# Performance work log

Measured on AMD Instinct MI355X. Metric: run time of the kernel, lower is better.

## Reference

```python
import jax, jax.numpy as jnp
import numpy as np

IN_DIM = 128
DIM = 32
N_HEADS = 4
EPS = 1e-5


def setup_inputs() -> dict:
    key = jax.random.key(0)
    ks = jax.random.split(key, 8)
    b, L = 1, 320
    s = 0.02
    return {
        "z": jax.random.normal(ks[0], (b, L, L, IN_DIM), dtype=jnp.float32),
        "ln_g": jnp.ones((IN_DIM,), jnp.float32),
        "ln_b": jnp.zeros((IN_DIM,), jnp.float32),
        "Wqkv": jax.random.normal(ks[1], (IN_DIM, DIM * 3 * N_HEADS), jnp.float32) * s,
        "Wpair": jax.random.normal(ks[2], (IN_DIM, N_HEADS), jnp.float32) * s,
        "Wgate": jax.random.normal(ks[3], (IN_DIM, N_HEADS * DIM), jnp.float32) * s,
        "bgate": jnp.zeros((N_HEADS * DIM,), jnp.float32),
        "Wout": jax.random.normal(ks[4], (N_HEADS * DIM, IN_DIM), jnp.float32) * s,
        "bout": jnp.zeros((IN_DIM,), jnp.float32),
    }


def _layernorm(x, g, b):
    m = jnp.mean(x, axis=-1, keepdims=True)
    v = jnp.mean(jnp.square(x - m), axis=-1, keepdims=True)
    return (x - m) * jax.lax.rsqrt(v + EPS) * g + b


def reference(z, ln_g, ln_b, Wqkv, Wpair, Wgate, bgate, Wout, bout):
    B, L, _, _ = z.shape
    zn = _layernorm(z, ln_g, ln_b)  # [b,i,j,c]
    qkv = zn @ Wqkv                 # [b,i,j,3*h*d]
    q, k, v = jnp.split(qkv, 3, axis=-1)
    rs = lambda t: t.reshape(B, L, L, N_HEADS, DIM)
    q, k, v = rs(q), rs(k), rs(v)
    pair_bias = zn @ Wpair          # [b,i,j,h]
    gate = jax.nn.sigmoid(zn @ Wgate + bgate)  # [b,i,j,h*d]
    scale = DIM ** 0.5
    # row-wise: attend over j within each row r=i
    # scores: [b,r,i,j,h]; bias broadcast over r
    scores = jnp.einsum('brihd,brjhd->brijh', q, k / scale)
    scores = scores + pair_bias[:, None]
    attn = jax.nn.softmax(scores, axis=3)
    out = jnp.einsum('brijh,brjhd->brihd', attn, v)  # [b,r,i,h,d]
    out = out.reshape(B, L, L, N_HEADS * DIM)
    return (gate * out) @ Wout + bout
```

## Files before the change

kernel.cpp:

```cpp
#include <hip/hip_runtime.h>
#include <math.h>


#define LL 320
#define CC 128
#define NPOS (LL*LL)

typedef __attribute__((ext_vector_type(8))) __bf16 bf16x8;
typedef __attribute__((ext_vector_type(4))) __bf16 bf16x4;
typedef __attribute__((ext_vector_type(4))) float f32x4;

#define MFMA16(a,b,c) __builtin_amdgcn_mfma_f32_16x16x32_bf16(a,b,c,0,0,0)

__device__ __forceinline__ int swz(int m, int kc) {
    return m*128 + ((kc ^ (m & 7)) << 3);
}

__global__ __launch_bounds__(128) void k_wprep(
    const float* __restrict__ Wqkv, const float* __restrict__ Wgate,
    const float* __restrict__ Wout, __bf16* __restrict__ wT)
{
    const int n = blockIdx.x, t = threadIdx.x;
    float v;
    if (n < 384)      v = Wqkv[(size_t)t*384 + n] * (n < 128 ? 0.17677669529663687f : 1.f);
    else if (n < 512) v = Wgate[(size_t)t*128 + (n-384)];
    else              v = Wout[(size_t)t*128 + (n-512)];
    wT[(size_t)n*128 + t] = (__bf16)v;
}

__global__ __launch_bounds__(512) void k_ln_proj(
    const float* __restrict__ z, const float* __restrict__ lng, const float* __restrict__ lnb,
    const __bf16* __restrict__ wT, const float* __restrict__ Wpair,
    const float* __restrict__ bgate,
    __bf16* __restrict__ qkvb, float* __restrict__ pairT, float* __restrict__ gate)
{
    __shared__ __bf16 As[128*128];
    __shared__ __bf16 Bs[128*128];
    const int t = threadIdx.x;
    const int posBase = blockIdx.x * 128;

    {
        const int r0 = t >> 2, q = t & 3;
        const float* zp = z + (size_t)(posBase + r0)*CC + q*32;
        float v[32];
        float s = 0.f, sq = 0.f;
#pragma unroll
        for (int i = 0; i < 8; ++i) {
            float4 f = ((const float4*)zp)[i];
            v[4*i+0]=f.x; v[4*i+1]=f.y; v[4*i+2]=f.z; v[4*i+3]=f.w;
            s  += f.x + f.y + f.z + f.w;
            sq += f.x*f.x + f.y*f.y + f.z*f.z + f.w*f.w;
        }
        s  += __shfl_xor(s, 1);  sq += __shfl_xor(sq, 1);
        s  += __shfl_xor(s, 2);  sq += __shfl_xor(sq, 2);
        const float mean = s * (1.f/128.f);
        const float var  = sq * (1.f/128.f) - mean*mean;
        const float rstd = rsqrtf(var + 1e-5f);
        const float4* g4 = (const float4*)(lng + q*32);
        const float4* b4 = (const float4*)(lnb + q*32);
#pragma unroll
        for (int i = 0; i < 8; ++i) {
            float4 gg = g4[i], bb = b4[i];
            v[4*i+0] = (v[4*i+0]-mean)*rstd*gg.x + bb.x;
            v[4*i+1] = (v[4*i+1]-mean)*rstd*gg.y + bb.y;
            v[4*i+2] = (v[4*i+2]-mean)*rstd*gg.z + bb.z;
            v[4*i+3] = (v[4*i+3]-mean)*rstd*gg.w + bb.w;
        }
#pragma unroll
        for (int i2 = 0; i2 < 8; ++i2) {
            bf16x4 pk;
            pk[0] = (__bf16)v[4*i2+0]; pk[1] = (__bf16)v[4*i2+1];
            pk[2] = (__bf16)v[4*i2+2]; pk[3] = (__bf16)v[4*i2+3];
            *(bf16x4*)&As[swz(r0, q*4 + (i2>>1)) + (i2&1)*4] = pk;
        }
        float pc0=0.f, pc1=0.f, pc2=0.f, pc3=0.f;
#pragma unroll 8
        for (int kk = 0; kk < 32; ++kk) {
            float4 wp = *(const float4*)&Wpair[(q*32 + kk)*4];
            pc0 += v[kk]*wp.x; pc1 += v[kk]*wp.y; pc2 += v[kk]*wp.z; pc3 += v[kk]*wp.w;
        }
        pc0 += __shfl_xor(pc0,1); pc0 += __shfl_xor(pc0,2);
        pc1 += __shfl_xor(pc1,1); pc1 += __shfl_xor(pc1,2);
        pc2 += __shfl_xor(pc2,1); pc2 += __shfl_xor(pc2,2);
        pc3 += __shfl_xor(pc3,1); pc3 += __shfl_xor(pc3,2);
        if (q == 0) {
            pairT[0*(size_t)NPOS + posBase + r0] = pc0;
            pairT[1*(size_t)NPOS + posBase + r0] = pc1;
            pairT[2*(size_t)NPOS + posBase + r0] = pc2;
            pairT[3*(size_t)NPOS + posBase + r0] = pc3;
        }
    }

    const int lane = t & 63, wv = t >> 6;
    const int l15 = lane & 15, quad = lane >> 4;
    const int m0 = wv * 16;
    const int srow = t >> 2, skc0 = (t & 3) * 4;

    for (int ch = 0; ch < 4; ++ch) {
        __syncthreads();
        {
            const __bf16* src = wT + (size_t)(ch*128 + srow)*128;
#pragma unroll
            for (int j = 0; j < 4; ++j)
                *(bf16x8*)&Bs[swz(srow, skc0 + j)] = *(const bf16x8*)(src + (skc0 + j)*8);
        }
        __syncthreads();

        f32x4 acc[8] = {};
#pragma unroll
        for (int kstep = 0; kstep < 4; ++kstep) {
            bf16x8 aA = *(const bf16x8*)&As[swz(m0 + l15, kstep*4 + quad)];
#pragma unroll
            for (int nt = 0; nt < 8; ++nt) {
                bf16x8 bB = *(const bf16x8*)&Bs[swz(nt*16 + l15, kstep*4 + quad)];
                acc[nt] = MFMA16(aA, bB, acc[nt]);
            }
        }

        if (ch < 3) {
#pragma unroll
            for (int reg = 0; reg < 4; ++reg) {
                __bf16* qp = qkvb + (size_t)(posBase + m0 + quad*4 + reg)*384 + ch*128 + l15;
#pragma unroll
                for (int nt = 0; nt < 8; ++nt)
                    qp[nt*16] = (__bf16)acc[nt][reg];
            }
        } else {
#pragma unroll
            for (int reg = 0; reg < 4; ++reg) {
                float* gp = gate + (size_t)(posBase + m0 + quad*4 + reg)*128 + l15;
#pragma unroll
                for (int nt = 0; nt < 8; ++nt) {
                    float x = acc[nt][reg] + bgate[nt*16 + l15];
                    gp[nt*16] = 1.f/(1.f + __expf(-x));
                }
            }
        }
    }
}

__global__ __launch_bounds__(256) void k_attn(
    const __bf16* __restrict__ qkvb, const float* __restrict__ pairT,
    const float* __restrict__ gate, __bf16* __restrict__ attb)
{
    __shared__ __bf16 Ks[64*32];
    __shared__ __bf16 Vt[32*72];
    __shared__ __bf16 Ps[4][16*72];

    const int t = threadIdx.x, wave = t >> 6, lane = t & 63;
    const int l15 = lane & 15, quad = lane >> 4;
    const int bx = blockIdx.x, r = bx / 5, itile = bx - r*5, h = blockIdx.y;
    const int iw0 = itile*64 + wave*16;

    bf16x8 aq = *(const bf16x8*)(qkvb + (size_t)(r*LL + iw0 + l15)*384 + h*32 + quad*8);

    f32x4 o0 = {0.f,0.f,0.f,0.f}, o1 = {0.f,0.f,0.f,0.f};
    float lp[4] = {0.f,0.f,0.f,0.f};
    const float* bp = pairT + (size_t)h*NPOS + (size_t)(iw0 + quad*4)*LL + l15;

    const int srow = t >> 2, sq4 = t & 3;
    const __bf16* kvbase = qkvb + (size_t)(r*LL)*384 + h*32 + sq4*8;
    __bf16* pw = &Ps[wave][0];

    for (int j0 = 0; j0 < LL; j0 += 64) {
        __syncthreads();
        {
            const __bf16* kp = kvbase + (size_t)(j0 + srow)*384 + 128;
            *(bf16x8*)&Ks[srow*32 + sq4*8] = *(const bf16x8*)kp;
            bf16x8 vv = *(const bf16x8*)(kp + 128);
#pragma unroll
            for (int i = 0; i < 8; ++i) Vt[(sq4*8 + i)*72 + srow] = vv[i];
        }
        __syncthreads();

        const f32x4 zero = {0.f,0.f,0.f,0.f};
        f32x4 s[4];
#pragma unroll
        for (int nt = 0; nt < 4; ++nt) {
            bf16x8 bk = *(const bf16x8*)&Ks[(nt*16 + l15)*32 + quad*8];
            s[nt] = MFMA16(aq, bk, zero);
        }
#pragma unroll
        for (int reg = 0; reg < 4; ++reg) {
            const float* bpr = bp + (size_t)reg*LL + j0;
            float rs = 0.f;
#pragma unroll
            for (int nt = 0; nt < 4; ++nt) {
                float p = __expf(s[nt][reg] + bpr[nt*16]);
                s[nt][reg] = p;
                rs += p;
            }
            lp[reg] += rs;
        }
#pragma unroll
        for (int reg = 0; reg < 4; ++reg)
#pragma unroll
            for (int nt = 0; nt < 4; ++nt)
                pw[(quad*4 + reg)*72 + nt*16 + l15] = (__bf16)s[nt][reg];

#pragma unroll
        for (int kk = 0; kk < 2; ++kk) {
            bf16x8 ap  = *(const bf16x8*)&pw[l15*72 + kk*32 + quad*8];
            bf16x8 bv0 = *(const bf16x8*)&Vt[(l15     )*72 + kk*32 + quad*8];
            bf16x8 bv1 = *(const bf16x8*)&Vt[(16 + l15)*72 + kk*32 + quad*8];
            o0 = MFMA16(ap, bv0, o0);
            o1 = MFMA16(ap, bv1, o1);
        }
    }

#pragma unroll
    for (int reg = 0; reg < 4; ++reg) {
        float x = lp[reg];
        x += __shfl_xor(x, 1); x += __shfl_xor(x, 2);
        x += __shfl_xor(x, 4); x += __shfl_xor(x, 8);
        const float inv = 1.f / x;
        const size_t pos = (size_t)(r*LL + iw0 + quad*4 + reg);
        const float* gp = gate + pos*128 + h*32 + l15;
        __bf16* op = attb + pos*128 + h*32 + l15;
        op[0]  = (__bf16)(o0[reg] * inv * gp[0]);
        op[16] = (__bf16)(o1[reg] * inv * gp[16]);
    }
}

__global__ __launch_bounds__(512) void k_out(
    const __bf16* __restrict__ attb, const __bf16* __restrict__ wT,
    const float* __restrict__ bout, float* __restrict__ out)
{
    __shared__ __bf16 As[128*128];
    __shared__ __bf16 Bs[128*128];
    const int t = threadIdx.x;
    const int posBase = blockIdx.x * 128;
    const int srow = t >> 2, skc0 = (t & 3) * 4;

    {
        const __bf16* asrc = attb + (size_t)(posBase + srow)*128;
        const __bf16* bsrc = wT + (size_t)(512 + srow)*128;
#pragma unroll
        for (int j = 0; j < 4; ++j) {
            *(bf16x8*)&As[swz(srow, skc0 + j)] = *(const bf16x8*)(asrc + (skc0 + j)*8);
            *(bf16x8*)&Bs[swz(srow, skc0 + j)] = *(const bf16x8*)(bsrc + (skc0 + j)*8);
        }
    }
    __syncthreads();

    const int lane = t & 63, wv = t >> 6;
    const int l15 = lane & 15, quad = lane >> 4;
    const int m0 = wv * 16;

    f32x4 acc[8] = {};
#pragma unroll
    for (int kstep = 0; kstep < 4; ++kstep) {
        bf16x8 aA = *(const bf16x8*)&As[swz(m0 + l15, kstep*4 + quad)];
#pragma unroll
        for (int nt = 0; nt < 8; ++nt) {
            bf16x8 bB = *(const bf16x8*)&Bs[swz(nt*16 + l15, kstep*4 + quad)];
            acc[nt] = MFMA16(aA, bB, acc[nt]);
        }
    }

#pragma unroll
    for (int reg = 0; reg < 4; ++reg) {
        float* op = out + (size_t)(posBase + m0 + quad*4 + reg)*128 + l15;
#pragma unroll
        for (int nt = 0; nt < 8; ++nt)
            op[nt*16] = acc[nt][reg] + bout[nt*16 + l15];
    }
}

extern "C" void kernel_launch(void* const* d_in, const int* in_sizes, int n_in,
                              void* d_out, int out_size, void* d_ws, size_t ws_size,
                              hipStream_t stream) {
    const float* z     = (const float*)d_in[0];
    const float* ln_g  = (const float*)d_in[1];
    const float* ln_b  = (const float*)d_in[2];
    const float* Wqkv  = (const float*)d_in[3];
    const float* Wpair = (const float*)d_in[4];
    const float* Wgate = (const float*)d_in[5];
    const float* bgate = (const float*)d_in[6];
    const float* Wout  = (const float*)d_in[7];
    const float* bout  = (const float*)d_in[8];
    float* out = (float*)d_out;

    __bf16* qkvb = (__bf16*)d_ws;
    __bf16* attb = qkvb + (size_t)NPOS*384;
    __bf16* wT   = attb + (size_t)NPOS*128;
    float*  gate = (float*)(wT + 640*128);
    float*  pairT = gate + (size_t)NPOS*128;

    k_wprep<<<640, 128, 0, stream>>>(Wqkv, Wgate, Wout, wT);
    k_ln_proj<<<800, 512, 0, stream>>>(z, ln_g, ln_b, wT, Wpair, bgate, qkvb, pairT, gate);
    k_attn<<<dim3(1600, 4), 256, 0, stream>>>(qkvb, pairT, gate, attb);
    k_out<<<800, 512, 0, stream>>>(attb, wT, bout, out);
}
```

Before: 310.4 us.

## Load full row K/V once per block and store gate and bias in bf16

The attention kernel now uses one block per (row, head). It holds all 320 keys and the transposed values in shared memory once, and each of its 5 waves processes 64 queries, computing transposed score tiles (K x Q) without the per-tile syncthreads loop. Before, each block reloaded K/V in 64-key chunks for only 64 queries. Separately, the gate and pair-bias intermediates are written and read as bf16 instead of fp32, which halves that memory traffic at some cost in precision. The larger shared memory footprint and 320-thread blocks may reduce occupancy.

New measurement: 295.0 us. 5.0% less time.

```diff
diff --git a/kernel.cpp b/kernel.cpp
--- a/kernel.cpp
+++ b/kernel.cpp
@@ -32,7 +32,7 @@
     const float* __restrict__ z, const float* __restrict__ lng, const float* __restrict__ lnb,
     const __bf16* __restrict__ wT, const float* __restrict__ Wpair,
     const float* __restrict__ bgate,
-    __bf16* __restrict__ qkvb, float* __restrict__ pairT, float* __restrict__ gate)
+    __bf16* __restrict__ qkvb, __bf16* __restrict__ biasb, __bf16* __restrict__ gateb)
 {
     __shared__ __bf16 As[128*128];
     __shared__ __bf16 Bs[128*128];
@@ -84,10 +84,10 @@
         pc2 += __shfl_xor(pc2,1); pc2 += __shfl_xor(pc2,2);
         pc3 += __shfl_xor(pc3,1); pc3 += __shfl_xor(pc3,2);
         if (q == 0) {
-            pairT[0*(size_t)NPOS + posBase + r0] = pc0;
-            pairT[1*(size_t)NPOS + posBase + r0] = pc1;
-            pairT[2*(size_t)NPOS + posBase + r0] = pc2;
-            pairT[3*(size_t)NPOS + posBase + r0] = pc3;
+            biasb[0*(size_t)NPOS + posBase + r0] = (__bf16)pc0;
+            biasb[1*(size_t)NPOS + posBase + r0] = (__bf16)pc1;
+            biasb[2*(size_t)NPOS + posBase + r0] = (__bf16)pc2;
+            biasb[3*(size_t)NPOS + posBase + r0] = (__bf16)pc3;
         }
     }
 
@@ -128,97 +128,124 @@
         } else {
 #pragma unroll
             for (int reg = 0; reg < 4; ++reg) {
-                float* gp = gate + (size_t)(posBase + m0 + quad*4 + reg)*128 + l15;
+                __bf16* gp = gateb + (size_t)(posBase + m0 + quad*4 + reg)*128 + l15;
 #pragma unroll
                 for (int nt = 0; nt < 8; ++nt) {
                     float x = acc[nt][reg] + bgate[nt*16 + l15];
-                    gp[nt*16] = 1.f/(1.f + __expf(-x));
+                    gp[nt*16] = (__bf16)(1.f/(1.f + __expf(-x)));
                 }
             }
         }
     }
 }
 
-__global__ __launch_bounds__(256) void k_attn(
-    const __bf16* __restrict__ qkvb, const float* __restrict__ pairT,
-    const float* __restrict__ gate, __bf16* __restrict__ attb)
+#define KS_ST 40
+#define VT_ST 328
+#define PW_ST 40
+__global__ __launch_bounds__(320) void k_attn(
+    const __bf16* __restrict__ qkvb, const __bf16* __restrict__ biasb,
+    const __bf16* __restrict__ gateb, __bf16* __restrict__ attb)
 {
-    __shared__ __bf16 Ks[64*32];
-    __shared__ __bf16 Vt[32*72];
-    __shared__ __bf16 Ps[4][16*72];
-
-    const int t = threadIdx.x, wave = t >> 6, lane = t & 63;
+    __shared__ __bf16 Ks[320*KS_ST];
+    __shared__ __bf16 Vt[32*VT_ST];
+    __shared__ __bf16 Pw[5*64*PW_ST];
+
+    const int t = threadIdx.x, wave = t / 64, lane = t & 63;
     const int l15 = lane & 15, quad = lane >> 4;
-    const int bx = blockIdx.x, r = bx / 5, itile = bx - r*5, h = blockIdx.y;
-    const int iw0 = itile*64 + wave*16;
-
-    bf16x8 aq = *(const bf16x8*)(qkvb + (size_t)(r*LL + iw0 + l15)*384 + h*32 + quad*8);
-
-    f32x4 o0 = {0.f,0.f,0.f,0.f}, o1 = {0.f,0.f,0.f,0.f};
+    const int r = blockIdx.x, h = blockIdx.y;
+    const int i0 = wave * 64;
+    const size_t rowBase = (size_t)r * LL;
+
+    {
+        const __bf16* kp = qkvb + (rowBase + t)*384 + 128 + h*32;
+#pragma unroll
+        for (int c = 0; c < 4; ++c)
+            *(bf16x8*)&Ks[t*KS_ST + c*8] = *(const bf16x8*)(kp + c*8);
+#pragma unroll
+        for (int c = 0; c < 4; ++c) {
+            bf16x8 vv = *(const bf16x8*)(kp + 128 + c*8);
+#pragma unroll
+            for (int e = 0; e < 8; ++e)
+                Vt[(c*8 + e)*VT_ST + t] = vv[e];
+        }
+    }
+
+    bf16x8 qf[4];
+#pragma unroll
+    for (int nt = 0; nt < 4; ++nt)
+        qf[nt] = *(const bf16x8*)(qkvb + (rowBase + i0 + nt*16 + l15)*384 + h*32 + quad*8);
+
+    __syncthreads();
+
+    f32x4 O[4][2] = {};
     float lp[4] = {0.f,0.f,0.f,0.f};
-    const float* bp = pairT + (size_t)h*NPOS + (size_t)(iw0 + quad*4)*LL + l15;
-
-    const int srow = t >> 2, sq4 = t & 3;
-    const __bf16* kvbase = qkvb + (size_t)(r*LL)*384 + h*32 + sq4*8;
-    __bf16* pw = &Ps[wave][0];
-
-    for (int j0 = 0; j0 < LL; j0 += 64) {
-        __syncthreads();
-        {
-            const __bf16* kp = kvbase + (size_t)(j0 + srow)*384 + 128;
-            *(bf16x8*)&Ks[srow*32 + sq4*8] = *(const bf16x8*)kp;
-            bf16x8 vv = *(const bf16x8*)(kp + 128);
-#pragma unroll
-            for (int i = 0; i < 8; ++i) Vt[(sq4*8 + i)*72 + srow] = vv[i];
-        }
-        __syncthreads();
-
+    __bf16* pw = &Pw[wave*64*PW_ST];
+    const __bf16* bbase = biasb + (size_t)h*NPOS;
+
+    for (int j0 = 0; j0 < LL; j0 += 32) {
         const f32x4 zero = {0.f,0.f,0.f,0.f};
-        f32x4 s[4];
+        bf16x8 kf[2];
+#pragma unroll
+        for (int mt = 0; mt < 2; ++mt)
+            kf[mt] = *(const bf16x8*)&Ks[(j0 + mt*16 + l15)*KS_ST + quad*8];
+        f32x4 st[2][4];
+#pragma unroll
+        for (int mt = 0; mt < 2; ++mt)
+#pragma unroll
+            for (int nt = 0; nt < 4; ++nt)
+                st[mt][nt] = MFMA16(kf[mt], qf[nt], zero);
+
 #pragma unroll
         for (int nt = 0; nt < 4; ++nt) {
-            bf16x8 bk = *(const bf16x8*)&Ks[(nt*16 + l15)*32 + quad*8];
-            s[nt] = MFMA16(aq, bk, zero);
-        }
+            const size_t bi = (size_t)(i0 + nt*16 + l15)*LL + j0;
+#pragma unroll
+            for (int mt = 0; mt < 2; ++mt) {
+                bf16x4 bb = *(const bf16x4*)(bbase + bi + mt*16 + quad*4);
+                bf16x4 pk;
+                float rs = 0.f;
+#pragma unroll
+                for (int reg = 0; reg < 4; ++reg) {
+                    float p = __expf(st[mt][nt][reg] + (float)bb[reg]);
+                    pk[reg] = (__bf16)p;
+                    rs += p;
+                }
+                lp[nt] += rs;
+                *(bf16x4*)&pw[(nt*16 + l15)*PW_ST + mt*16 + quad*4] = pk;
+            }
+        }
+
+        bf16x8 vf[2];
+#pragma unroll
+        for (int dt = 0; dt < 2; ++dt)
+            vf[dt] = *(const bf16x8*)&Vt[(dt*16 + l15)*VT_ST + j0 + quad*8];
+#pragma unroll
+        for (int nt = 0; nt < 4; ++nt) {
+            bf16x8 pf = *(const bf16x8*)&pw[(nt*16 + l15)*PW_ST + quad*8];
+#pragma unroll
+            for (int dt = 0; dt < 2; ++dt)
+                O[nt][dt] = MFMA16(pf, vf[dt], O[nt][dt]);
+        }
+    }
+
+#pragma unroll
+    for (int nt = 0; nt < 4; ++nt) {
+        lp[nt] += __shfl_xor(lp[nt], 16);
+        lp[nt] += __shfl_xor(lp[nt], 32);
+    }
+#pragma unroll
+    for (int nt = 0; nt < 4; ++nt) {
 #pragma unroll
         for (int reg = 0; reg < 4; ++reg) {
-            const float* bpr = bp + (size_t)reg*LL + j0;
-            float rs = 0.f;
-#pragma unroll
-            for (int nt = 0; nt < 4; ++nt) {
-                float p = __expf(s[nt][reg] + bpr[nt*16]);
-                s[nt][reg] = p;
-                rs += p;
-            }
-            lp[reg] += rs;
-        }
-#pragma unroll
-        for (int reg = 0; reg < 4; ++reg)
-#pragma unroll
-            for (int nt = 0; nt < 4; ++nt)
-                pw[(quad*4 + reg)*72 + nt*16 + l15] = (__bf16)s[nt][reg];
-
-#pragma unroll
-        for (int kk = 0; kk < 2; ++kk) {
-            bf16x8 ap  = *(const bf16x8*)&pw[l15*72 + kk*32 + quad*8];
-            bf16x8 bv0 = *(const bf16x8*)&Vt[(l15     )*72 + kk*32 + quad*8];
-            bf16x8 bv1 = *(const bf16x8*)&Vt[(16 + l15)*72 + kk*32 + quad*8];
-            o0 = MFMA16(ap, bv0, o0);
-            o1 = MFMA16(ap, bv1, o1);
-        }
-    }
-
-#pragma unroll
-    for (int reg = 0; reg < 4; ++reg) {
-        float x = lp[reg];
-        x += __shfl_xor(x, 1); x += __shfl_xor(x, 2);
-        x += __shfl_xor(x, 4); x += __shfl_xor(x, 8);
-        const float inv = 1.f / x;
-        const size_t pos = (size_t)(r*LL + iw0 + quad*4 + reg);
-        const float* gp = gate + pos*128 + h*32 + l15;
-        __bf16* op = attb + pos*128 + h*32 + l15;
-        op[0]  = (__bf16)(o0[reg] * inv * gp[0]);
-        op[16] = (__bf16)(o1[reg] * inv * gp[16]);
+            const float lsum = __shfl(lp[nt], quad*4 + reg);
+            const float inv = 1.f / lsum;
+            const size_t pos = rowBase + i0 + nt*16 + quad*4 + reg;
+#pragma unroll
+            for (int dt = 0; dt < 2; ++dt) {
+                const int d = dt*16 + l15;
+                const float g = (float)gateb[pos*128 + h*32 + d];
+                attb[pos*128 + h*32 + d] = (__bf16)(O[nt][dt][reg] * inv * g);
+            }
+        }
     }
 }
 
@@ -281,14 +308,14 @@
     const float* bout  = (const float*)d_in[8];
     float* out = (float*)d_out;
 
-    __bf16* qkvb = (__bf16*)d_ws;
-    __bf16* attb = qkvb + (size_t)NPOS*384;
-    __bf16* wT   = attb + (size_t)NPOS*128;
-    float*  gate = (float*)(wT + 640*128);
-    float*  pairT = gate + (size_t)NPOS*128;
+    __bf16* qkvb  = (__bf16*)d_ws;
+    __bf16* attb  = qkvb  + (size_t)NPOS*384;
+    __bf16* wT    = attb  + (size_t)NPOS*128;
+    __bf16* gateb = wT    + (size_t)640*128;
+    __bf16* biasb = gateb + (size_t)NPOS*128;
 
     k_wprep<<<640, 128, 0, stream>>>(Wqkv, Wgate, Wout, wT);
-    k_ln_proj<<<800, 512, 0, stream>>>(z, ln_g, ln_b, wT, Wpair, bgate, qkvb, pairT, gate);
-    k_attn<<<dim3(1600, 4), 256, 0, stream>>>(qkvb, pairT, gate, attb);
+    k_ln_proj<<<800, 512, 0, stream>>>(z, ln_g, ln_b, wT, Wpair, bgate, qkvb, biasb, gateb);
+    k_attn<<<dim3(320, 4), 320, 0, stream>>>(qkvb, biasb, gateb, attb);
     k_out<<<800, 512, 0, stream>>>(attb, wT, bout, out);
 }
```
